# Kernel optimization log

Hardware: AMD Instinct MI355X
Metric: run time of the kernel (lower is better)

The kernel has to match this reference:

```python
import jax, jax.numpy as jnp
import numpy as np
import math

D_MODEL = 1024
N_HEADS = 16
HEAD_DIM = 64
BATCH = 2
SEQ = 2048


def setup_inputs() -> dict:
    key = jax.random.key(0)
    ks = jax.random.split(key, 5)
    x = jax.random.normal(ks[0], (BATCH, SEQ, D_MODEL), dtype=jnp.float32)
    s = 0.02
    wq = jax.random.normal(ks[1], (D_MODEL, D_MODEL), dtype=jnp.float32) * s
    wk = jax.random.normal(ks[2], (D_MODEL, D_MODEL), dtype=jnp.float32) * s
    wv = jax.random.normal(ks[3], (D_MODEL, D_MODEL), dtype=jnp.float32) * s
    wo = jax.random.normal(ks[4], (D_MODEL, D_MODEL), dtype=jnp.float32) * s
    gammas = jnp.linspace(0.9, 0.99, N_HEADS, dtype=jnp.float32)
    return {"x": x, "wq": wq, "wk": wk, "wv": wv, "wo": wo, "gammas": gammas}


def _decay_mask(length: int, gammas: jnp.ndarray, dtype) -> jnp.ndarray:
    # [H, L, L]: gamma^(t-s) for t >= s, else 0 (causal exponential decay)
    pos = jnp.arange(length)
    diff = pos[:, None] - pos[None, :]
    causal = diff >= 0
    d = jnp.maximum(diff, 0).astype(dtype)
    g = gammas.astype(dtype)[:, None, None]
    return jnp.where(causal[None], jnp.power(g, d[None]), jnp.zeros((), dtype))


def reference(x, wq, wk, wv, wo, gammas):
    B, L, D = x.shape
    H, hd = N_HEADS, HEAD_DIM
    # torch nn.Linear: y = x @ W.T
    q = (x @ wq.T).reshape(B, L, H, hd)
    k = (x @ wk.T).reshape(B, L, H, hd)
    v = (x @ wv.T).reshape(B, L, H, hd)
    scale = 1.0 / math.sqrt(hd)
    scores = jnp.einsum('bthd,bshd->bhts', q * scale, k)  # [B,H,L,L]
    decay = _decay_mask(L, gammas, x.dtype)               # [H,L,L]
    weights = scores * decay[None]
    retained = jnp.einsum('bhts,bshd->bthd', weights, v)  # [B,L,H,hd]
    return retained.reshape(B, L, H * hd) @ wo.T
```

## Files before the change

kernel.cpp:

```cpp
#include <hip/hip_runtime.h>


typedef __attribute__((ext_vector_type(8))) short bf16x8;
typedef __attribute__((ext_vector_type(4))) float f32x4;
typedef __attribute__((ext_vector_type(16))) float f32x16;
typedef __attribute__((ext_vector_type(4))) unsigned short u16x4;
typedef __attribute__((ext_vector_type(8))) unsigned short u16x8;
typedef __attribute__((ext_vector_type(4))) unsigned int u32x4;

__device__ inline unsigned short f2bf(float f) {
    unsigned int u;
    __builtin_memcpy(&u, &f, 4);
    u += 0x7fffu + ((u >> 16) & 1u);
    return (unsigned short)(u >> 16);
}

__device__ inline f32x4 mfma16(bf16x8 a, bf16x8 b, f32x4 c) {
    return __builtin_amdgcn_mfma_f32_16x16x32_bf16(a, b, c, 0, 0, 0);
}
__device__ inline f32x16 mfma32(bf16x8 a, bf16x8 b, f32x16 c) {
    return __builtin_amdgcn_mfma_f32_32x32x16_bf16(a, b, c, 0, 0, 0);
}

__device__ inline void gl16(const unsigned short* g, unsigned short* l) {
    __builtin_amdgcn_global_load_lds(
        (const __attribute__((address_space(1))) unsigned int*)g,
        (__attribute__((address_space(3))) unsigned int*)l,
        16, 0, 0);
}

__device__ inline unsigned cvtpk(float lo, float hi) {
    unsigned r;
    asm("v_cvt_pk_bf16_f32 %0, %1, %2" : "=v"(r) : "v"(lo), "v"(hi));
    return r;
}

__global__ __launch_bounds__(256) void convert_bf16(
    const float* __restrict__ x,
    const float* __restrict__ wq, const float* __restrict__ wk,
    const float* __restrict__ wv, const float* __restrict__ wo,
    unsigned short* __restrict__ xb,
    unsigned short* __restrict__ wqb, unsigned short* __restrict__ wkb,
    unsigned short* __restrict__ wvb, unsigned short* __restrict__ wob)
{
    int cid = blockIdx.x * 256 + threadIdx.x;
    #pragma unroll
    for (int it = 0; it < 4; ++it, cid += 262144) {
        const float* src;
        unsigned short* dst;
        size_t off;
        if (cid < 524288) {
            src = x; dst = xb; off = (size_t)cid * 8;
        } else {
            const int t = cid - 524288;
            const int seg = t >> 17;
            off = (size_t)(t & 131071) * 8;
            src = seg == 0 ? wq : seg == 1 ? wk : seg == 2 ? wv : wo;
            dst = seg == 0 ? wqb : seg == 1 ? wkb : seg == 2 ? wvb : wob;
        }
        f32x4 a = *(const f32x4*)(src + off);
        f32x4 b = *(const f32x4*)(src + off + 4);
        u32x4 v = { cvtpk(a[0], a[1]), cvtpk(a[2], a[3]),
                    cvtpk(b[0], b[1]), cvtpk(b[2], b[3]) };
        *(u32x4*)(dst + off) = v;
    }
}

__global__ __launch_bounds__(256) void qkv_bf16(
    const unsigned short* __restrict__ xb,
    const unsigned short* __restrict__ wqb, const unsigned short* __restrict__ wkb,
    const unsigned short* __restrict__ wvb,
    unsigned short* __restrict__ qfr, unsigned short* __restrict__ kfr,
    unsigned short* __restrict__ vfr)
{
    __shared__ unsigned short sR[128 * 64];
    __shared__ unsigned short sL[128 * 64];

    const int z = blockIdx.z;
    const unsigned short* W = (z == 0) ? wqb : (z == 1) ? wkb : wvb;
    const unsigned short* Rs = (z < 2) ? xb : W;
    const unsigned short* Ls = (z < 2) ? W : xb;
    const int rblk = (z < 2) ? blockIdx.x : blockIdx.y;
    const int lblk = (z < 2) ? blockIdx.y : blockIdx.x;

    const int tid = threadIdx.x;
    const int l = tid & 63, w = tid >> 6;
    const int lrow = l & 15, koff4 = (l >> 4) * 4;
    const int swz = lrow & 7;
    const int wrow = (w >> 1) * 64, wcol = (w & 1) * 64;

    f32x4 acc[4][4] = {};

    const int srow = w * 32 + (l >> 3);
    const int scol = ((l & 7) ^ ((l >> 3) & 7)) * 8;
    const unsigned short* gR = Rs + (size_t)(rblk * 128 + srow) * 1024 + scol;
    const unsigned short* gL = Ls + (size_t)(lblk * 128 + srow) * 1024 + scol;
    unsigned short* lRb = sR + (w * 32) * 64;
    unsigned short* lLb = sL + (w * 32) * 64;

    for (int kk = 0; kk < 1024; kk += 64) {
        #pragma unroll
        for (int p = 0; p < 4; ++p) {
            gl16(gR + (size_t)p * 8 * 1024 + kk, lRb + p * 512);
            gl16(gL + (size_t)p * 8 * 1024 + kk, lLb + p * 512);
        }
        __syncthreads();
        #pragma unroll
        for (int kt = 0; kt < 2; ++kt) {
            bf16x8 aL[4], bR[4];
            #pragma unroll
            for (int f = 0; f < 4; ++f) {
                const int co = ((kt * 4 + (l >> 4)) ^ swz) * 8;
                aL[f] = *(const bf16x8*)&sL[(wcol + f * 16 + lrow) * 64 + co];
                bR[f] = *(const bf16x8*)&sR[(wrow + f * 16 + lrow) * 64 + co];
            }
            #pragma unroll
            for (int af = 0; af < 4; ++af)
                #pragma unroll
                for (int bf = 0; bf < 4; ++bf)
                    acc[af][bf] = mfma16(aL[af], bR[bf], acc[af][bf]);
        }
        __syncthreads();
    }

    #pragma unroll
    for (int af = 0; af < 4; ++af) {
        #pragma unroll
        for (int bf = 0; bf < 4; ++bf) {
            const int m = rblk * 128 + wrow + bf * 16 + lrow;
            const int n0 = lblk * 128 + wcol + af * 16 + koff4;
            f32x4 v = acc[af][bf];
            unsigned p0 = cvtpk(v[0], v[1]), p1 = cvtpk(v[2], v[3]);
            u16x4 val = { (unsigned short)(p0 & 0xffff), (unsigned short)(p0 >> 16),
                          (unsigned short)(p1 & 0xffff), (unsigned short)(p1 >> 16) };
            if (z < 2) {
                const int bq = m >> 11, s = m & 2047;
                const int h2 = n0 >> 6, dd = n0 & 63;
                const size_t addr = (size_t)((bq * 16 + h2) * 64 + (s >> 5)) * 2048
                                  + (size_t)(dd >> 4) * 512 + (size_t)((dd >> 3) & 1) * 256
                                  + (size_t)(s & 31) * 8 + (dd & 7);
                unsigned short* dst = z ? kfr : qfr;
                *(u16x4*)(dst + addr) = val;
            } else {
                const int h2 = m >> 6, dd = m & 63;
                const int bq = n0 >> 11, t = n0 & 2047;
                const size_t addr = (size_t)((bq * 16 + h2) * 64 + (t >> 5)) * 2048
                                  + (size_t)((dd >> 5) * 2 + ((t >> 4) & 1)) * 512
                                  + (size_t)((t >> 3) & 1) * 256
                                  + (size_t)(dd & 31) * 8 + (t & 7);
                *(u16x4*)(vfr + addr) = val;
            }
        }
    }
}

__global__ __launch_bounds__(256) void retention_single(
    const unsigned short* __restrict__ qfr, const unsigned short* __restrict__ kfr,
    const unsigned short* __restrict__ vfr, const float* __restrict__ gammas,
    unsigned short* __restrict__ ret)
{
    __shared__ float red[3][32][64];

    const int bid = blockIdx.x;
    const int xcd = bid & 7;
    const int r_ = bid >> 3;
    const int p = r_ >> 2;
    const int m = r_ & 3;
    const int tw = 63 - p;
    const int b = m >> 1;
    const int pi = b ? (7 - xcd) : xcd;
    const int h = (m & 1) ? (15 - pi) : pi;
    const float lg = log2f(gammas[h]);
    const int cut_i = (int)(45.0f / (-lg));
    const float gi32 = exp2f(-32.0f * lg);

    const int tid = threadIdx.x;
    const int l = tid & 63, w = tid >> 6;
    const int l31 = l & 31, hi = l >> 5;
    const int tw0 = tw << 5;
    const int tq = tw0 + l31;

    const size_t hbase = (size_t)((b * 16 + h) * 64) * 2048;
    const unsigned short* qfb = qfr + hbase + l * 8;
    const unsigned short* kfb = kfr + hbase + l * 8;
    const unsigned short* vfb = vfr + hbase + l * 8;

    bf16x8 qf[4];
    #pragma unroll
    for (int kt = 0; kt < 4; ++kt)
        qf[kt] = *(const bf16x8*)(qfb + (size_t)tw * 2048 + kt * 512);

    float cf[16];
    #pragma unroll
    for (int r = 0; r < 16; ++r) {
        const int crow = (r & 3) + (hi << 2) + ((r >> 2) << 3);
        cf[r] = exp2f((float)(31 - crow) * lg);
    }

    int sb_lo = tw0 - 31 - cut_i;
    sb_lo = (sb_lo <= 0) ? 0 : (sb_lo >> 5);

    const int n = tw - sb_lo + 1;
    const int chunk = (n + 3) >> 2;
    const int my_lo = sb_lo + w * chunk;
    int my_hi = my_lo + chunk;
    if (my_hi > tw + 1) my_hi = tw + 1;

    f32x16 acc0 = {}, acc1 = {};

    if (my_lo < my_hi) {
        float rowf = 0.125f * exp2f((float)(tq - (my_lo << 5) - 31) * lg);

        bf16x8 kA[4], vA[4], kB[4], vB[4];

        auto load = [&](int sb, bf16x8* kf, bf16x8* vf) {
            const unsigned short* kp = kfb + (size_t)sb * 2048;
            const unsigned short* vp = vfb + (size_t)sb * 2048;
            #pragma unroll
            for (int kt = 0; kt < 4; ++kt) kf[kt] = *(const bf16x8*)(kp + kt * 512);
            #pragma unroll
            for (int i = 0; i < 4; ++i) vf[i] = *(const bf16x8*)(vp + i * 512);
        };

        auto compute = [&](const bf16x8* kc, const bf16x8* vc, int sb) {
            f32x16 sc = {};
            __builtin_amdgcn_s_setprio(1);
            #pragma unroll
            for (int kt = 0; kt < 4; ++kt) sc = mfma32(kc[kt], qf[kt], sc);
            __builtin_amdgcn_s_setprio(0);

            float wv_[16];
            if (sb == tw) {
                const int dtq = tq - (sb << 5);
                #pragma unroll
                for (int r = 0; r < 16; ++r) {
                    const int crow = (r & 3) + (hi << 2) + ((r >> 2) << 3);
                    float t_ = sc[r] * rowf * cf[r];
                    wv_[r] = (dtq >= crow) ? t_ : 0.0f;
                }
            } else {
                #pragma unroll
                for (int r = 0; r < 16; ++r)
                    wv_[r] = sc[r] * rowf * cf[r];
            }
            unsigned pk_[8];
            #pragma unroll
            for (int i = 0; i < 8; ++i) pk_[i] = cvtpk(wv_[2 * i], wv_[2 * i + 1]);
            asm("v_permlane32_swap_b32 %0, %1" : "+v"(pk_[0]), "+v"(pk_[2]));
            asm("v_permlane32_swap_b32 %0, %1" : "+v"(pk_[1]), "+v"(pk_[3]));
            asm("v_permlane32_swap_b32 %0, %1" : "+v"(pk_[4]), "+v"(pk_[6]));
            asm("v_permlane32_swap_b32 %0, %1" : "+v"(pk_[5]), "+v"(pk_[7]));
            u32x4 f0v = { pk_[0], pk_[1], pk_[2], pk_[3] };
            u32x4 f1v = { pk_[4], pk_[5], pk_[6], pk_[7] };
            const bf16x8 pa0 = __builtin_bit_cast(bf16x8, f0v);
            const bf16x8 pa1 = __builtin_bit_cast(bf16x8, f1v);
            __builtin_amdgcn_s_setprio(1);
            acc0 = mfma32(pa0, vc[0], acc0);
            acc0 = mfma32(pa1, vc[1], acc0);
            acc1 = mfma32(pa0, vc[2], acc1);
            acc1 = mfma32(pa1, vc[3], acc1);
            __builtin_amdgcn_s_setprio(0);
            rowf *= gi32;
        };

        int sb = my_lo;
        load(sb, kA, vA);
        while (true) {
            const bool moreB = (sb + 1 < my_hi);
            if (moreB) load(sb + 1, kB, vB);
            compute(kA, vA, sb);
            ++sb;
            if (!moreB) break;
            const bool moreA = (sb + 1 < my_hi);
            if (moreA) load(sb + 1, kA, vA);
            compute(kB, vB, sb);
            ++sb;
            if (!moreA) break;
        }
    }

    if (w > 0) {
        #pragma unroll
        for (int r = 0; r < 16; ++r) {
            red[w - 1][r][l]      = acc0[r];
            red[w - 1][r + 16][l] = acc1[r];
        }
    }
    __syncthreads();
    if (w == 0) {
        #pragma unroll
        for (int jj = 0; jj < 3; ++jj)
            #pragma unroll
            for (int r = 0; r < 16; ++r) {
                acc0[r] += red[jj][r][l];
                acc1[r] += red[jj][r + 16][l];
            }
        #pragma unroll
        for (int r = 0; r < 16; ++r) {
            const int tl = (r & 3) + (hi << 2) + ((r >> 2) << 3);
            unsigned short* dst = ret + (size_t)(b * 2048 + tw0 + tl) * 1024 + h * 64 + l31;
            dst[0]  = f2bf(acc0[r]);
            dst[32] = f2bf(acc1[r]);
        }
    }
}

__global__ __launch_bounds__(256) void out_bf16(
    const unsigned short* __restrict__ ret, const unsigned short* __restrict__ wob,
    float* __restrict__ out)
{
    __shared__ unsigned short sR[128 * 64];
    __shared__ unsigned short sL[128 * 64];

    const int rblk = blockIdx.x;
    const int lblk = blockIdx.y;

    const int tid = threadIdx.x;
    const int l = tid & 63, w = tid >> 6;
    const int lrow = l & 15, koff4 = (l >> 4) * 4;
    const int swz = lrow & 7;
    const int wrow = (w >> 1) * 64, wcol = (w & 1) * 64;

    f32x4 acc[4][4] = {};

    const int srow = w * 32 + (l >> 3);
    const int scol = ((l & 7) ^ ((l >> 3) & 7)) * 8;
    const unsigned short* gR = ret + (size_t)(rblk * 128 + srow) * 1024 + scol;
    const unsigned short* gL = wob + (size_t)(lblk * 128 + srow) * 1024 + scol;
    unsigned short* lRb = sR + (w * 32) * 64;
    unsigned short* lLb = sL + (w * 32) * 64;

    for (int kk = 0; kk < 1024; kk += 64) {
        #pragma unroll
        for (int p = 0; p < 4; ++p) {
            gl16(gR + (size_t)p * 8 * 1024 + kk, lRb + p * 512);
            gl16(gL + (size_t)p * 8 * 1024 + kk, lLb + p * 512);
        }
        __syncthreads();
        #pragma unroll
        for (int kt = 0; kt < 2; ++kt) {
            bf16x8 aL[4], bR[4];
            #pragma unroll
            for (int f = 0; f < 4; ++f) {
                const int co = ((kt * 4 + (l >> 4)) ^ swz) * 8;
                aL[f] = *(const bf16x8*)&sL[(wcol + f * 16 + lrow) * 64 + co];
                bR[f] = *(const bf16x8*)&sR[(wrow + f * 16 + lrow) * 64 + co];
            }
            #pragma unroll
            for (int af = 0; af < 4; ++af)
                #pragma unroll
                for (int bf = 0; bf < 4; ++bf)
                    acc[af][bf] = mfma16(aL[af], bR[bf], acc[af][bf]);
        }
        __syncthreads();
    }

    #pragma unroll
    for (int af = 0; af < 4; ++af)
        #pragma unroll
        for (int bf = 0; bf < 4; ++bf) {
            const int m = rblk * 128 + wrow + bf * 16 + lrow;
            const int n0 = lblk * 128 + wcol + af * 16 + koff4;
            *(f32x4*)(out + (size_t)m * 1024 + n0) = acc[af][bf];
        }
}

extern "C" void kernel_launch(void* const* d_in, const int* in_sizes, int n_in,
                              void* d_out, int out_size, void* d_ws, size_t ws_size,
                              hipStream_t stream) {
    const float* x      = (const float*)d_in[0];
    const float* wq     = (const float*)d_in[1];
    const float* wk     = (const float*)d_in[2];
    const float* wv     = (const float*)d_in[3];
    const float* wo     = (const float*)d_in[4];
    const float* gammas = (const float*)d_in[5];
    float* out = (float*)d_out;

    unsigned short* ws = (unsigned short*)d_ws;
    unsigned short* qf  = ws;
    unsigned short* kf  = ws + (size_t)4 * 1024 * 1024;
    unsigned short* vf  = ws + (size_t)8 * 1024 * 1024;
    unsigned short* ret = ws + (size_t)12 * 1024 * 1024;
    unsigned short* xb  = ret;
    unsigned short* wqb = ws + (size_t)16 * 1024 * 1024;
    unsigned short* wkb = ws + (size_t)17 * 1024 * 1024;
    unsigned short* wvb = ws + (size_t)18 * 1024 * 1024;
    unsigned short* wob = ws + (size_t)19 * 1024 * 1024;

    convert_bf16<<<1024, 256, 0, stream>>>(x, wq, wk, wv, wo, xb, wqb, wkb, wvb, wob);
    qkv_bf16<<<dim3(32, 8, 3), 256, 0, stream>>>(xb, wqb, wkb, wvb, qf, kf, vf);
    retention_single<<<2048, 256, 0, stream>>>(qf, kf, vf, gammas, ret);
    out_bf16<<<dim3(32, 8), 256, 0, stream>>>(ret, wob, out);
}
```

Baseline: 93.28 us.

## Stage K/V tiles through LDS with async loads and fold decay into K

The retention kernel now streams each wave's K and V blocks into a per-wave double-buffered LDS region with direct global-to-LDS loads and explicit vmcnt waits, where it used to keep register double buffers. The per-column decay factor gamma^(31-s) is folded into K during the QKV projection epilogue, which removes the per-element cf multiply in the inner loop. The reduction buffer reuses the K/V LDS space, and the block-to-batch mapping is rotated to spread work across XCDs. This is meant to cut register pressure and hide load latency, at the cost of extra LDS traffic and some bf16 rounding of the scaled K.

Measured after the change: 106.1 us. 1.14x slower.

```diff
diff --git a/kernel.cpp b/kernel.cpp
--- a/kernel.cpp
+++ b/kernel.cpp
@@ -69,7 +69,7 @@
 __global__ __launch_bounds__(256) void qkv_bf16(
     const unsigned short* __restrict__ xb,
     const unsigned short* __restrict__ wqb, const unsigned short* __restrict__ wkb,
-    const unsigned short* __restrict__ wvb,
+    const unsigned short* __restrict__ wvb, const float* __restrict__ gammas,
     unsigned short* __restrict__ qfr, unsigned short* __restrict__ kfr,
     unsigned short* __restrict__ vfr)
 {
@@ -130,6 +130,11 @@
             const int m = rblk * 128 + wrow + bf * 16 + lrow;
             const int n0 = lblk * 128 + wcol + af * 16 + koff4;
             f32x4 v = acc[af][bf];
+            if (z == 1) {
+                const float lgh = log2f(gammas[(n0 >> 6) & 15]);
+                const float sf = exp2f(lgh * (float)(31 - (m & 31)));
+                v[0] *= sf; v[1] *= sf; v[2] *= sf; v[3] *= sf;
+            }
             unsigned p0 = cvtpk(v[0], v[1]), p1 = cvtpk(v[2], v[3]);
             u16x4 val = { (unsigned short)(p0 & 0xffff), (unsigned short)(p0 >> 16),
                           (unsigned short)(p1 & 0xffff), (unsigned short)(p1 >> 16) };
@@ -154,18 +159,18 @@
     }
 }
 
-__global__ __launch_bounds__(256) void retention_single(
+__global__ __launch_bounds__(256) void retention_lds(
     const unsigned short* __restrict__ qfr, const unsigned short* __restrict__ kfr,
     const unsigned short* __restrict__ vfr, const float* __restrict__ gammas,
     unsigned short* __restrict__ ret)
 {
-    __shared__ float red[3][32][64];
+    __shared__ unsigned short kv[4][2][4096];
 
     const int bid = blockIdx.x;
     const int xcd = bid & 7;
     const int r_ = bid >> 3;
     const int p = r_ >> 2;
-    const int m = r_ & 3;
+    const int m = ((r_ & 3) + (r_ >> 5)) & 3;
     const int tw = 63 - p;
     const int b = m >> 1;
     const int pi = b ? (7 - xcd) : xcd;
@@ -190,13 +195,6 @@
     for (int kt = 0; kt < 4; ++kt)
         qf[kt] = *(const bf16x8*)(qfb + (size_t)tw * 2048 + kt * 512);
 
-    float cf[16];
-    #pragma unroll
-    for (int r = 0; r < 16; ++r) {
-        const int crow = (r & 3) + (hi << 2) + ((r >> 2) << 3);
-        cf[r] = exp2f((float)(31 - crow) * lg);
-    }
-
     int sb_lo = tw0 - 31 - cut_i;
     sb_lo = (sb_lo <= 0) ? 0 : (sb_lo >> 5);
 
@@ -206,23 +204,38 @@
     int my_hi = my_lo + chunk;
     if (my_hi > tw + 1) my_hi = tw + 1;
 
+    unsigned short* slot[2] = { &kv[w][0][0], &kv[w][1][0] };
+
+    auto stage = [&](int sb, unsigned short* s) {
+        const unsigned short* kp = kfb + (size_t)sb * 2048;
+        const unsigned short* vp = vfb + (size_t)sb * 2048;
+        #pragma unroll
+        for (int t = 0; t < 4; ++t) gl16(kp + t * 512, s + t * 512);
+        #pragma unroll
+        for (int t = 0; t < 4; ++t) gl16(vp + t * 512, s + 2048 + t * 512);
+    };
+
     f32x16 acc0 = {}, acc1 = {};
 
     if (my_lo < my_hi) {
         float rowf = 0.125f * exp2f((float)(tq - (my_lo << 5) - 31) * lg);
-
-        bf16x8 kA[4], vA[4], kB[4], vB[4];
-
-        auto load = [&](int sb, bf16x8* kf, bf16x8* vf) {
-            const unsigned short* kp = kfb + (size_t)sb * 2048;
-            const unsigned short* vp = vfb + (size_t)sb * 2048;
-            #pragma unroll
-            for (int kt = 0; kt < 4; ++kt) kf[kt] = *(const bf16x8*)(kp + kt * 512);
-            #pragma unroll
-            for (int i = 0; i < 4; ++i) vf[i] = *(const bf16x8*)(vp + i * 512);
-        };
-
-        auto compute = [&](const bf16x8* kc, const bf16x8* vc, int sb) {
+        stage(my_lo, slot[0]);
+        if (my_lo + 1 < my_hi) stage(my_lo + 1, slot[1]);
+
+        for (int sb = my_lo; sb < my_hi; ++sb) {
+            unsigned short* cur = slot[(sb - my_lo) & 1];
+            if (sb + 1 < my_hi) asm volatile("s_waitcnt vmcnt(8)" ::: "memory");
+            else                asm volatile("s_waitcnt vmcnt(0)" ::: "memory");
+            __builtin_amdgcn_sched_barrier(0);
+
+            bf16x8 kc[4], vc[4];
+            #pragma unroll
+            for (int kt = 0; kt < 4; ++kt)
+                kc[kt] = *(const bf16x8*)(cur + kt * 512 + l * 8);
+            #pragma unroll
+            for (int i = 0; i < 4; ++i)
+                vc[i] = *(const bf16x8*)(cur + 2048 + i * 512 + l * 8);
+
             f32x16 sc = {};
             __builtin_amdgcn_s_setprio(1);
             #pragma unroll
@@ -235,13 +248,13 @@
                 #pragma unroll
                 for (int r = 0; r < 16; ++r) {
                     const int crow = (r & 3) + (hi << 2) + ((r >> 2) << 3);
-                    float t_ = sc[r] * rowf * cf[r];
+                    float t_ = sc[r] * rowf;
                     wv_[r] = (dtq >= crow) ? t_ : 0.0f;
                 }
             } else {
                 #pragma unroll
                 for (int r = 0; r < 16; ++r)
-                    wv_[r] = sc[r] * rowf * cf[r];
+                    wv_[r] = sc[r] * rowf;
             }
             unsigned pk_[8];
             #pragma unroll
@@ -261,29 +274,22 @@
             acc1 = mfma32(pa1, vc[3], acc1);
             __builtin_amdgcn_s_setprio(0);
             rowf *= gi32;
-        };
-
-        int sb = my_lo;
-        load(sb, kA, vA);
-        while (true) {
-            const bool moreB = (sb + 1 < my_hi);
-            if (moreB) load(sb + 1, kB, vB);
-            compute(kA, vA, sb);
-            ++sb;
-            if (!moreB) break;
-            const bool moreA = (sb + 1 < my_hi);
-            if (moreA) load(sb + 1, kA, vA);
-            compute(kB, vB, sb);
-            ++sb;
-            if (!moreA) break;
-        }
-    }
-
+
+            if (sb + 2 < my_hi) {
+                asm volatile("s_waitcnt lgkmcnt(0)" ::: "memory");
+                __builtin_amdgcn_sched_barrier(0);
+                stage(sb + 2, cur);
+            }
+        }
+    }
+
+    __syncthreads();
+    float* red = (float*)&kv[0][0][0];
     if (w > 0) {
         #pragma unroll
         for (int r = 0; r < 16; ++r) {
-            red[w - 1][r][l]      = acc0[r];
-            red[w - 1][r + 16][l] = acc1[r];
+            red[(w - 1) * 2048 + r * 64 + l]        = acc0[r];
+            red[(w - 1) * 2048 + (r + 16) * 64 + l] = acc1[r];
         }
     }
     __syncthreads();
@@ -292,8 +298,8 @@
         for (int jj = 0; jj < 3; ++jj)
             #pragma unroll
             for (int r = 0; r < 16; ++r) {
-                acc0[r] += red[jj][r][l];
-                acc1[r] += red[jj][r + 16][l];
+                acc0[r] += red[jj * 2048 + r * 64 + l];
+                acc1[r] += red[jj * 2048 + (r + 16) * 64 + l];
             }
         #pragma unroll
         for (int r = 0; r < 16; ++r) {
@@ -388,7 +394,7 @@
     unsigned short* wob = ws + (size_t)19 * 1024 * 1024;
 
     convert_bf16<<<1024, 256, 0, stream>>>(x, wq, wk, wv, wo, xb, wqb, wkb, wvb, wob);
-    qkv_bf16<<<dim3(32, 8, 3), 256, 0, stream>>>(xb, wqb, wkb, wvb, qf, kf, vf);
-    retention_single<<<2048, 256, 0, stream>>>(qf, kf, vf, gammas, ret);
+    qkv_bf16<<<dim3(32, 8, 3), 256, 0, stream>>>(xb, wqb, wkb, wvb, gammas, qf, kf, vf);
+    retention_lds<<<2048, 256, 0, stream>>>(qf, kf, vf, gammas, ret);
     out_bf16<<<dim3(32, 8), 256, 0, stream>>>(ret, wob, out);
 }
```

## Process two query tiles per retention block and prefetch GEMM K-tiles

Applied to the files above, without the earlier changes.

The retention kernel now handles two adjacent 32-row query tiles per block, so each K/V tile loaded from memory is reused for both score computations, and the grid is halved. The two projection GEMMs move the global-to-LDS stage of the next K slice to right after the fragment reads, so it overlaps the MFMA work, and they raise wave priority during the MFMAs. The retention change adds register pressure (two Q fragment sets and four accumulators) and a two-phase reduction with extra barriers. It also cuts the number of blocks available for load balancing across the causal triangle.

Result: slower. 96.82 us (+3.8%).

```diff
diff --git a/kernel.cpp b/kernel.cpp
--- a/kernel.cpp
+++ b/kernel.cpp
@@ -98,29 +98,45 @@
     unsigned short* lRb = sR + (w * 32) * 64;
     unsigned short* lLb = sL + (w * 32) * 64;
 
-    for (int kk = 0; kk < 1024; kk += 64) {
+    auto stage = [&](int kk) {
         #pragma unroll
         for (int p = 0; p < 4; ++p) {
             gl16(gR + (size_t)p * 8 * 1024 + kk, lRb + p * 512);
             gl16(gL + (size_t)p * 8 * 1024 + kk, lLb + p * 512);
         }
-        __syncthreads();
-        #pragma unroll
-        for (int kt = 0; kt < 2; ++kt) {
-            bf16x8 aL[4], bR[4];
+    };
+
+    stage(0);
+    for (int kk = 0; kk < 1024; kk += 64) {
+        asm volatile("s_waitcnt vmcnt(0)" ::: "memory");
+        __builtin_amdgcn_s_barrier();
+        __builtin_amdgcn_sched_barrier(0);
+
+        bf16x8 aL[2][4], bR[2][4];
+        #pragma unroll
+        for (int kt = 0; kt < 2; ++kt)
             #pragma unroll
             for (int f = 0; f < 4; ++f) {
                 const int co = ((kt * 4 + (l >> 4)) ^ swz) * 8;
-                aL[f] = *(const bf16x8*)&sL[(wcol + f * 16 + lrow) * 64 + co];
-                bR[f] = *(const bf16x8*)&sR[(wrow + f * 16 + lrow) * 64 + co];
-            }
+                aL[kt][f] = *(const bf16x8*)&sL[(wcol + f * 16 + lrow) * 64 + co];
+                bR[kt][f] = *(const bf16x8*)&sR[(wrow + f * 16 + lrow) * 64 + co];
+            }
+        asm volatile("s_waitcnt lgkmcnt(0)" ::: "memory");
+        __builtin_amdgcn_sched_barrier(0);
+        __builtin_amdgcn_s_barrier();
+        __builtin_amdgcn_sched_barrier(0);
+
+        if (kk + 64 < 1024) stage(kk + 64);
+
+        __builtin_amdgcn_s_setprio(1);
+        #pragma unroll
+        for (int kt = 0; kt < 2; ++kt)
             #pragma unroll
             for (int af = 0; af < 4; ++af)
                 #pragma unroll
                 for (int bf = 0; bf < 4; ++bf)
-                    acc[af][bf] = mfma16(aL[af], bR[bf], acc[af][bf]);
-        }
-        __syncthreads();
+                    acc[af][bf] = mfma16(aL[kt][af], bR[kt][bf], acc[af][bf]);
+        __builtin_amdgcn_s_setprio(0);
     }
 
     #pragma unroll
@@ -154,7 +170,7 @@
     }
 }
 
-__global__ __launch_bounds__(256) void retention_single(
+__global__ __launch_bounds__(256) void retention_twin(
     const unsigned short* __restrict__ qfr, const unsigned short* __restrict__ kfr,
     const unsigned short* __restrict__ vfr, const float* __restrict__ gammas,
     unsigned short* __restrict__ ret)
@@ -164,31 +180,34 @@
     const int bid = blockIdx.x;
     const int xcd = bid & 7;
     const int r_ = bid >> 3;
-    const int p = r_ >> 2;
+    const int pr = 31 - (r_ >> 2);
     const int m = r_ & 3;
-    const int tw = 63 - p;
+    const int tA = pr << 1, tB = tA + 1;
     const int b = m >> 1;
     const int pi = b ? (7 - xcd) : xcd;
     const int h = (m & 1) ? (15 - pi) : pi;
     const float lg = log2f(gammas[h]);
     const int cut_i = (int)(45.0f / (-lg));
     const float gi32 = exp2f(-32.0f * lg);
+    const float g32 = exp2f(32.0f * lg);
 
     const int tid = threadIdx.x;
     const int l = tid & 63, w = tid >> 6;
     const int l31 = l & 31, hi = l >> 5;
-    const int tw0 = tw << 5;
-    const int tq = tw0 + l31;
+    const int tA0 = tA << 5, tB0 = tB << 5;
+    const int tqA = tA0 + l31;
 
     const size_t hbase = (size_t)((b * 16 + h) * 64) * 2048;
     const unsigned short* qfb = qfr + hbase + l * 8;
     const unsigned short* kfb = kfr + hbase + l * 8;
     const unsigned short* vfb = vfr + hbase + l * 8;
 
-    bf16x8 qf[4];
-    #pragma unroll
-    for (int kt = 0; kt < 4; ++kt)
-        qf[kt] = *(const bf16x8*)(qfb + (size_t)tw * 2048 + kt * 512);
+    bf16x8 qfA[4], qfB[4];
+    #pragma unroll
+    for (int kt = 0; kt < 4; ++kt) {
+        qfA[kt] = *(const bf16x8*)(qfb + (size_t)tA * 2048 + kt * 512);
+        qfB[kt] = *(const bf16x8*)(qfb + (size_t)tB * 2048 + kt * 512);
+    }
 
     float cf[16];
     #pragma unroll
@@ -197,21 +216,21 @@
         cf[r] = exp2f((float)(31 - crow) * lg);
     }
 
-    int sb_lo = tw0 - 31 - cut_i;
-    sb_lo = (sb_lo <= 0) ? 0 : (sb_lo >> 5);
-
-    const int n = tw - sb_lo + 1;
+    int lo = tA0 - 31 - cut_i;
+    lo = (lo <= 0) ? 0 : (lo >> 5);
+
+    const int n = tB - lo + 1;
     const int chunk = (n + 3) >> 2;
-    const int my_lo = sb_lo + w * chunk;
+    const int my_lo = lo + w * chunk;
     int my_hi = my_lo + chunk;
-    if (my_hi > tw + 1) my_hi = tw + 1;
-
-    f32x16 acc0 = {}, acc1 = {};
+    if (my_hi > tB + 1) my_hi = tB + 1;
+
+    f32x16 aA0 = {}, aA1 = {}, aB0 = {}, aB1 = {};
 
     if (my_lo < my_hi) {
-        float rowf = 0.125f * exp2f((float)(tq - (my_lo << 5) - 31) * lg);
-
-        bf16x8 kA[4], vA[4], kB[4], vB[4];
+        float rowfA = 0.125f * exp2f((float)(tqA - (my_lo << 5) - 31) * lg);
+
+        bf16x8 k1[4], v1[4], k2[4], v2[4];
 
         auto load = [&](int sb, bf16x8* kf, bf16x8* vf) {
             const unsigned short* kp = kfb + (size_t)sb * 2048;
@@ -223,85 +242,130 @@
         };
 
         auto compute = [&](const bf16x8* kc, const bf16x8* vc, int sb) {
-            f32x16 sc = {};
+            const bool hasA = (sb <= tA);
+            f32x16 scA = {}, scB = {};
             __builtin_amdgcn_s_setprio(1);
-            #pragma unroll
-            for (int kt = 0; kt < 4; ++kt) sc = mfma32(kc[kt], qf[kt], sc);
+            if (hasA) {
+                #pragma unroll
+                for (int kt = 0; kt < 4; ++kt) scA = mfma32(kc[kt], qfA[kt], scA);
+            }
+            #pragma unroll
+            for (int kt = 0; kt < 4; ++kt) scB = mfma32(kc[kt], qfB[kt], scB);
             __builtin_amdgcn_s_setprio(0);
 
-            float wv_[16];
-            if (sb == tw) {
-                const int dtq = tq - (sb << 5);
+            const float rowfB = rowfA * g32;
+            if (hasA) {
+                float wv_[16];
+                if (sb == tA) {
+                    #pragma unroll
+                    for (int r = 0; r < 16; ++r) {
+                        const int crow = (r & 3) + (hi << 2) + ((r >> 2) << 3);
+                        float t_ = scA[r] * rowfA * cf[r];
+                        wv_[r] = (l31 >= crow) ? t_ : 0.0f;
+                    }
+                } else {
+                    #pragma unroll
+                    for (int r = 0; r < 16; ++r) wv_[r] = scA[r] * rowfA * cf[r];
+                }
+                unsigned pk_[8];
+                #pragma unroll
+                for (int i = 0; i < 8; ++i) pk_[i] = cvtpk(wv_[2 * i], wv_[2 * i + 1]);
+                asm("v_permlane32_swap_b32 %0, %1" : "+v"(pk_[0]), "+v"(pk_[2]));
+                asm("v_permlane32_swap_b32 %0, %1" : "+v"(pk_[1]), "+v"(pk_[3]));
+                asm("v_permlane32_swap_b32 %0, %1" : "+v"(pk_[4]), "+v"(pk_[6]));
+                asm("v_permlane32_swap_b32 %0, %1" : "+v"(pk_[5]), "+v"(pk_[7]));
+                u32x4 f0v = { pk_[0], pk_[1], pk_[2], pk_[3] };
+                u32x4 f1v = { pk_[4], pk_[5], pk_[6], pk_[7] };
+                const bf16x8 pa0 = __builtin_bit_cast(bf16x8, f0v);
+                const bf16x8 pa1 = __builtin_bit_cast(bf16x8, f1v);
+                __builtin_amdgcn_s_setprio(1);
+                aA0 = mfma32(pa0, vc[0], aA0);
+                aA0 = mfma32(pa1, vc[1], aA0);
+                aA1 = mfma32(pa0, vc[2], aA1);
+                aA1 = mfma32(pa1, vc[3], aA1);
+                __builtin_amdgcn_s_setprio(0);
+            }
+            {
+                float wv_[16];
+                if (sb == tB) {
+                    #pragma unroll
+                    for (int r = 0; r < 16; ++r) {
+                        const int crow = (r & 3) + (hi << 2) + ((r >> 2) << 3);
+                        float t_ = scB[r] * rowfB * cf[r];
+                        wv_[r] = (l31 >= crow) ? t_ : 0.0f;
+                    }
+                } else {
+                    #pragma unroll
+                    for (int r = 0; r < 16; ++r) wv_[r] = scB[r] * rowfB * cf[r];
+                }
+                unsigned pk_[8];
+                #pragma unroll
+                for (int i = 0; i < 8; ++i) pk_[i] = cvtpk(wv_[2 * i], wv_[2 * i + 1]);
+                asm("v_permlane32_swap_b32 %0, %1" : "+v"(pk_[0]), "+v"(pk_[2]));
+                asm("v_permlane32_swap_b32 %0, %1" : "+v"(pk_[1]), "+v"(pk_[3]));
+                asm("v_permlane32_swap_b32 %0, %1" : "+v"(pk_[4]), "+v"(pk_[6]));
+                asm("v_permlane32_swap_b32 %0, %1" : "+v"(pk_[5]), "+v"(pk_[7]));
+                u32x4 f0v = { pk_[0], pk_[1], pk_[2], pk_[3] };
+                u32x4 f1v = { pk_[4], pk_[5], pk_[6], pk_[7] };
+                const bf16x8 pb0 = __builtin_bit_cast(bf16x8, f0v);
+                const bf16x8 pb1 = __builtin_bit_cast(bf16x8, f1v);
+                __builtin_amdgcn_s_setprio(1);
+                aB0 = mfma32(pb0, vc[0], aB0);
+                aB0 = mfma32(pb1, vc[1], aB0);
+                aB1 = mfma32(pb0, vc[2], aB1);
+                aB1 = mfma32(pb1, vc[3], aB1);
+                __builtin_amdgcn_s_setprio(0);
+            }
+            rowfA *= gi32;
+        };
+
+        int sb = my_lo;
+        load(sb, k1, v1);
+        while (true) {
+            const bool more1 = (sb + 1 < my_hi);
+            if (more1) load(sb + 1, k2, v2);
+            compute(k1, v1, sb);
+            ++sb;
+            if (!more1) break;
+            const bool more2 = (sb + 1 < my_hi);
+            if (more2) load(sb + 1, k1, v1);
+            compute(k2, v2, sb);
+            ++sb;
+            if (!more2) break;
+        }
+    }
+
+    #pragma unroll
+    for (int phase = 0; phase < 2; ++phase) {
+        const f32x16& p0 = phase ? aB0 : aA0;
+        const f32x16& p1 = phase ? aB1 : aA1;
+        const int t0 = phase ? tB0 : tA0;
+        if (w > 0) {
+            #pragma unroll
+            for (int r = 0; r < 16; ++r) {
+                red[w - 1][r][l]      = p0[r];
+                red[w - 1][r + 16][l] = p1[r];
+            }
+        }
+        __syncthreads();
+        if (w == 0) {
+            f32x16 s0 = p0, s1 = p1;
+            #pragma unroll
+            for (int jj = 0; jj < 3; ++jj)
                 #pragma unroll
                 for (int r = 0; r < 16; ++r) {
-                    const int crow = (r & 3) + (hi << 2) + ((r >> 2) << 3);
-                    float t_ = sc[r] * rowf * cf[r];
-                    wv_[r] = (dtq >= crow) ? t_ : 0.0f;
+                    s0[r] += red[jj][r][l];
+                    s1[r] += red[jj][r + 16][l];
                 }
-            } else {
-                #pragma unroll
-                for (int r = 0; r < 16; ++r)
-                    wv_[r] = sc[r] * rowf * cf[r];
-            }
-            unsigned pk_[8];
-            #pragma unroll
-            for (int i = 0; i < 8; ++i) pk_[i] = cvtpk(wv_[2 * i], wv_[2 * i + 1]);
-            asm("v_permlane32_swap_b32 %0, %1" : "+v"(pk_[0]), "+v"(pk_[2]));
-            asm("v_permlane32_swap_b32 %0, %1" : "+v"(pk_[1]), "+v"(pk_[3]));
-            asm("v_permlane32_swap_b32 %0, %1" : "+v"(pk_[4]), "+v"(pk_[6]));
-            asm("v_permlane32_swap_b32 %0, %1" : "+v"(pk_[5]), "+v"(pk_[7]));
-            u32x4 f0v = { pk_[0], pk_[1], pk_[2], pk_[3] };
-            u32x4 f1v = { pk_[4], pk_[5], pk_[6], pk_[7] };
-            const bf16x8 pa0 = __builtin_bit_cast(bf16x8, f0v);
-            const bf16x8 pa1 = __builtin_bit_cast(bf16x8, f1v);
-            __builtin_amdgcn_s_setprio(1);
-            acc0 = mfma32(pa0, vc[0], acc0);
-            acc0 = mfma32(pa1, vc[1], acc0);
-            acc1 = mfma32(pa0, vc[2], acc1);
-            acc1 = mfma32(pa1, vc[3], acc1);
-            __builtin_amdgcn_s_setprio(0);
-            rowf *= gi32;
-        };
-
-        int sb = my_lo;
-        load(sb, kA, vA);
-        while (true) {
-            const bool moreB = (sb + 1 < my_hi);
-            if (moreB) load(sb + 1, kB, vB);
-            compute(kA, vA, sb);
-            ++sb;
-            if (!moreB) break;
-            const bool moreA = (sb + 1 < my_hi);
-            if (moreA) load(sb + 1, kA, vA);
-            compute(kB, vB, sb);
-            ++sb;
-            if (!moreA) break;
-        }
-    }
-
-    if (w > 0) {
-        #pragma unroll
-        for (int r = 0; r < 16; ++r) {
-            red[w - 1][r][l]      = acc0[r];
-            red[w - 1][r + 16][l] = acc1[r];
-        }
-    }
-    __syncthreads();
-    if (w == 0) {
-        #pragma unroll
-        for (int jj = 0; jj < 3; ++jj)
             #pragma unroll
             for (int r = 0; r < 16; ++r) {
-                acc0[r] += red[jj][r][l];
-                acc1[r] += red[jj][r + 16][l];
-            }
-        #pragma unroll
-        for (int r = 0; r < 16; ++r) {
-            const int tl = (r & 3) + (hi << 2) + ((r >> 2) << 3);
-            unsigned short* dst = ret + (size_t)(b * 2048 + tw0 + tl) * 1024 + h * 64 + l31;
-            dst[0]  = f2bf(acc0[r]);
-            dst[32] = f2bf(acc1[r]);
-        }
+                const int tl = (r & 3) + (hi << 2) + ((r >> 2) << 3);
+                unsigned short* dst = ret + (size_t)(b * 2048 + t0 + tl) * 1024 + h * 64 + l31;
+                dst[0]  = f2bf(s0[r]);
+                dst[32] = f2bf(s1[r]);
+            }
+        }
+        __syncthreads();
     }
 }
 
@@ -330,29 +394,45 @@
     unsigned short* lRb = sR + (w * 32) * 64;
     unsigned short* lLb = sL + (w * 32) * 64;
 
-    for (int kk = 0; kk < 1024; kk += 64) {
+    auto stage = [&](int kk) {
         #pragma unroll
         for (int p = 0; p < 4; ++p) {
             gl16(gR + (size_t)p * 8 * 1024 + kk, lRb + p * 512);
             gl16(gL + (size_t)p * 8 * 1024 + kk, lLb + p * 512);
         }
-        __syncthreads();
-        #pragma unroll
-        for (int kt = 0; kt < 2; ++kt) {
-            bf16x8 aL[4], bR[4];
+    };
+
+    stage(0);
+    for (int kk = 0; kk < 1024; kk += 64) {
+        asm volatile("s_waitcnt vmcnt(0)" ::: "memory");
+        __builtin_amdgcn_s_barrier();
+        __builtin_amdgcn_sched_barrier(0);
+
+        bf16x8 aL[2][4], bR[2][4];
+        #pragma unroll
+        for (int kt = 0; kt < 2; ++kt)
             #pragma unroll
             for (int f = 0; f < 4; ++f) {
                 const int co = ((kt * 4 + (l >> 4)) ^ swz) * 8;
-                aL[f] = *(const bf16x8*)&sL[(wcol + f * 16 + lrow) * 64 + co];
-                bR[f] = *(const bf16x8*)&sR[(wrow + f * 16 + lrow) * 64 + co];
-            }
+                aL[kt][f] = *(const bf16x8*)&sL[(wcol + f * 16 + lrow) * 64 + co];
+                bR[kt][f] = *(const bf16x8*)&sR[(wrow + f * 16 + lrow) * 64 + co];
+            }
+        asm volatile("s_waitcnt lgkmcnt(0)" ::: "memory");
+        __builtin_amdgcn_sched_barrier(0);
+        __builtin_amdgcn_s_barrier();
+        __builtin_amdgcn_sched_barrier(0);
+
+        if (kk + 64 < 1024) stage(kk + 64);
+
+        __builtin_amdgcn_s_setprio(1);
+        #pragma unroll
+        for (int kt = 0; kt < 2; ++kt)
             #pragma unroll
             for (int af = 0; af < 4; ++af)
                 #pragma unroll
                 for (int bf = 0; bf < 4; ++bf)
-                    acc[af][bf] = mfma16(aL[af], bR[bf], acc[af][bf]);
-        }
-        __syncthreads();
+                    acc[af][bf] = mfma16(aL[kt][af], bR[kt][bf], acc[af][bf]);
+        __builtin_amdgcn_s_setprio(0);
     }
 
     #pragma unroll
@@ -389,6 +469,6 @@
 
     convert_bf16<<<1024, 256, 0, stream>>>(x, wq, wk, wv, wo, xb, wqb, wkb, wvb, wob);
     qkv_bf16<<<dim3(32, 8, 3), 256, 0, stream>>>(xb, wqb, wkb, wvb, qf, kf, vf);
-    retention_single<<<2048, 256, 0, stream>>>(qf, kf, vf, gammas, ret);
+    retention_twin<<<1024, 256, 0, stream>>>(qf, kf, vf, gammas, ret);
     out_bf16<<<dim3(32, 8), 256, 0, stream>>>(ret, wob, out);
 }
```
